# Optimization experiments

Hardware: AMD Instinct MI355X
Metric: run time of the kernel (lower is better)

The kernel has to match this reference:

```python
import jax, jax.numpy as jnp
import numpy as np

N_PED = 131072      # total pedestrians (batch)
SEG = 64            # pedestrians per segment (equal-size groups)
N_SEQ = N_PED // SEG
D_IN = 256          # enc_h_dim
D_OUT = 128         # mlp_dim


def setup_inputs() -> dict:
    key = jax.random.key(0)
    k1, k2 = jax.random.split(key, 2)
    h_states = jax.random.normal(k1, (N_PED, D_IN), dtype=jnp.float32)
    W = jax.random.normal(k2, (D_IN, D_OUT), dtype=jnp.float32) * 0.05
    b = jnp.zeros((D_OUT,), dtype=jnp.float32)
    starts = jnp.arange(N_SEQ, dtype=jnp.int64) * SEG
    seq_start_end = jnp.stack([starts, starts + SEG], axis=1)  # [N_SEQ, 2]
    return {"h_states": h_states, "W": W, "b": b, "seq_start_end": seq_start_end}


def reference(h_states, W, b, seq_start_end):
    # fc projection: (N, D_IN) -> (N, D_OUT)
    h = h_states @ W + b
    # gather each segment: equal-size groups of SEG pedestrians
    starts = seq_start_end[:, 0]                     # [G]
    idx = starts[:, None] + jnp.arange(SEG)[None, :]  # [G, S]
    seg = h[idx]                                      # [G, S, D_OUT]
    # per-segment self-attention pooling: softmax(H H^T) @ H
    scores = jnp.einsum('gsd,gtd->gst', seg, seg)     # [G, S, S]
    attn = jax.nn.softmax(scores, axis=-1)
    ctx = jnp.einsum('gst,gtd->gsd', attn, seg)       # [G, S, D_OUT]
    return ctx.reshape(-1, D_OUT)                     # [N, D_OUT]
```

## Files before the change

kernel.cpp:

```cpp
#include <hip/hip_runtime.h>
#include <stdint.h>

#define SEG 64
#define D_IN 256
#define D_OUT 128
#define NSEQ 2048

typedef __attribute__((ext_vector_type(8))) _Float16 half8;
typedef __attribute__((ext_vector_type(4))) float floatx4;

static __device__ __forceinline__ unsigned short f2h_bits(float f) {
  union { _Float16 h; unsigned short u; } v; v.h = (_Float16)f; return v.u;
}

__global__ void prep_w_kernel(const float* __restrict__ W,
                              unsigned short* __restrict__ Wf) {
  const int idx = blockIdx.x * 256 + threadIdx.x;
  const float v = W[idx];
  const int k = idx >> 7, n = idx & 127;
  const int slot = (((n >> 4) * 8 + (k >> 5)) * 64 + ((n & 15) + 16 * ((k >> 3) & 3))) * 8 + (k & 7);
  Wf[slot] = f2h_bits(v);
}

struct SharedHT {
  unsigned short h[4][4][64][8];
  unsigned short ht[8][2][64][8];
};
union alignas(16) SharedU {
  unsigned short a[4][8][64][8];
  SharedHT s;
};

__global__ __launch_bounds__(256, 4)
void attn_fused(const float* __restrict__ hs,
                const unsigned short* __restrict__ Wf,
                const float* __restrict__ bias,
                float* __restrict__ out)
{
  __shared__ SharedU u;
  __shared__ float rowinv[SEG];

  const int g    = blockIdx.x;
  const int tid  = (int)threadIdx.x;
  const int w    = tid >> 6;
  const int lane = tid & 63;
  const int c    = lane & 15;
  const int q    = lane >> 4;

  {
    const float4* gsrc = (const float4*)(hs + (size_t)g * (SEG * D_IN));
#pragma unroll
    for (int i = 0; i < 16; ++i) {
      const int f = i * 256 + tid;
      const float4 v = gsrc[f];
      const int row = f >> 6, col0 = (f & 63) * 4;
      const unsigned lo = (unsigned)f2h_bits(v.x) | ((unsigned)f2h_bits(v.y) << 16);
      const unsigned hi = (unsigned)f2h_bits(v.z) | ((unsigned)f2h_bits(v.w) << 16);
      *(uint2*)(&u.a[row >> 4][col0 >> 5][(row & 15) + 16 * ((col0 >> 3) & 3)][col0 & 7]) =
          make_uint2(lo, hi);
    }
  }

  float bv[2];
#pragma unroll
  for (int nt = 0; nt < 2; ++nt) bv[nt] = bias[(2 * w + nt) * 16 + c];
  floatx4 acc[2][4];
#pragma unroll
  for (int nt = 0; nt < 2; ++nt)
#pragma unroll
    for (int mt = 0; mt < 4; ++mt)
      acc[nt][mt] = (floatx4){bv[nt], bv[nt], bv[nt], bv[nt]};

  __syncthreads();

  {
    const half8* WfV = (const half8*)Wf;
#pragma unroll
    for (int ks = 0; ks < 8; ++ks) {
      const half8 wf0 = WfV[((2 * w + 0) * 8 + ks) * 64 + lane];
      const half8 wf1 = WfV[((2 * w + 1) * 8 + ks) * 64 + lane];
      half8 af[4];
#pragma unroll
      for (int mt = 0; mt < 4; ++mt)
        af[mt] = *(const half8*)(&u.a[mt][ks][lane][0]);
#pragma unroll
      for (int mt = 0; mt < 4; ++mt) {
        acc[0][mt] = __builtin_amdgcn_mfma_f32_16x16x32_f16(af[mt], wf0, acc[0][mt], 0, 0, 0);
        acc[1][mt] = __builtin_amdgcn_mfma_f32_16x16x32_f16(af[mt], wf1, acc[1][mt], 0, 0, 0);
      }
    }
  }

  __syncthreads();

#pragma unroll
  for (int nt = 0; nt < 2; ++nt) {
    const int ntg = 2 * w + nt;
#pragma unroll
    for (int mt = 0; mt < 4; ++mt) {
      unsigned short hb[4];
#pragma unroll
      for (int i = 0; i < 4; ++i) hb[i] = f2h_bits(acc[nt][mt][i]);
      const int lph = 16 * ((2 * nt + (c >> 3)) & 3);
#pragma unroll
      for (int i = 0; i < 4; ++i)
        u.s.h[mt][w][4 * q + i + lph][c & 7] = hb[i];
      const int lanep = c + 16 * ((2 * mt + (q >> 1)) & 3);
      const unsigned lo = (unsigned)hb[0] | ((unsigned)hb[1] << 16);
      const unsigned hi = (unsigned)hb[2] | ((unsigned)hb[3] << 16);
      *(uint2*)(&u.s.ht[ntg][mt >> 1][lanep][(q & 1) * 4]) = make_uint2(lo, hi);
    }
  }

  __syncthreads();

  floatx4 sacc[4];
#pragma unroll
  for (int nt = 0; nt < 4; ++nt) sacc[nt] = (floatx4){0.f, 0.f, 0.f, 0.f};
#pragma unroll
  for (int ks = 0; ks < 4; ++ks) {
    const half8 a = *(const half8*)(&u.s.h[w][ks][lane][0]);
#pragma unroll
    for (int nt = 0; nt < 4; ++nt) {
      const half8 b = *(const half8*)(&u.s.h[nt][ks][lane][0]);
      sacc[nt] = __builtin_amdgcn_mfma_f32_16x16x32_f16(a, b, sacc[nt], 0, 0, 0);
    }
  }

  __syncthreads();

  unsigned short pb[4][4];
  float rs[4];
#pragma unroll
  for (int i = 0; i < 4; ++i) {
    float m = fmaxf(fmaxf(sacc[0][i], sacc[1][i]), fmaxf(sacc[2][i], sacc[3][i]));
#pragma unroll
    for (int d = 1; d < 16; d <<= 1) m = fmaxf(m, __shfl_xor(m, d, 64));
    float ssum = 0.f;
#pragma unroll
    for (int nt = 0; nt < 4; ++nt) {
      const float e = __expf(sacc[nt][i] - m);
      ssum += e;
      pb[i][nt] = f2h_bits(e);
    }
#pragma unroll
    for (int d = 1; d < 16; d <<= 1) ssum += __shfl_xor(ssum, d, 64);
    rs[i] = ssum;
  }

  unsigned short (*pfr)[2][64][8] = (unsigned short(*)[2][64][8])(&u.s.h[0][0][0][0]);
#pragma unroll
  for (int i = 0; i < 4; ++i)
#pragma unroll
    for (int nt = 0; nt < 4; ++nt)
      pfr[w][nt >> 1][4 * q + i + 16 * ((2 * nt + (c >> 3)) & 3)][c & 7] = pb[i][nt];
  if (c == 0) {
#pragma unroll
    for (int i = 0; i < 4; ++i)
      rowinv[16 * w + 4 * q + i] = 1.0f / rs[i];
  }

  __syncthreads();

  floatx4 cacc[4][2];
#pragma unroll
  for (int mt = 0; mt < 4; ++mt)
#pragma unroll
    for (int nn = 0; nn < 2; ++nn) cacc[mt][nn] = (floatx4){0.f, 0.f, 0.f, 0.f};
#pragma unroll
  for (int ks = 0; ks < 2; ++ks) {
    half8 bfr[2];
#pragma unroll
    for (int nn = 0; nn < 2; ++nn)
      bfr[nn] = *(const half8*)(&u.s.ht[2 * w + nn][ks][lane][0]);
#pragma unroll
    for (int mt = 0; mt < 4; ++mt) {
      const half8 a = *(const half8*)(&pfr[mt][ks][lane][0]);
#pragma unroll
      for (int nn = 0; nn < 2; ++nn)
        cacc[mt][nn] = __builtin_amdgcn_mfma_f32_16x16x32_f16(a, bfr[nn], cacc[mt][nn], 0, 0, 0);
    }
  }

  float* ob = out + (size_t)g * (SEG * D_OUT);
#pragma unroll
  for (int mt = 0; mt < 4; ++mt)
#pragma unroll
    for (int i = 0; i < 4; ++i) {
      const int s = 16 * mt + 4 * q + i;
      const float inv = rowinv[s];
#pragma unroll
      for (int nn = 0; nn < 2; ++nn)
        ob[s * D_OUT + 32 * w + 16 * nn + c] = cacc[mt][nn][i] * inv;
    }
}

extern "C" void kernel_launch(void* const* d_in, const int* in_sizes, int n_in,
                              void* d_out, int out_size, void* d_ws, size_t ws_size,
                              hipStream_t stream) {
  const float* hs   = (const float*)d_in[0];
  const float* W    = (const float*)d_in[1];
  const float* bias = (const float*)d_in[2];
  float* out = (float*)d_out;
  unsigned short* Wf = (unsigned short*)d_ws;

  prep_w_kernel<<<128, 256, 0, stream>>>(W, Wf);
  attn_fused<<<NSEQ, 256, 0, stream>>>(hs, Wf, bias, out);
}
```

Before: 222.5 us.

## Remove two barriers by keeping P@V per-wave with private softmax buffer

Each wave now does the P@V product for its own 16 query rows across all 128 output columns, using a private per-wave probability buffer. That removes the two block barriers around the softmax write and the rowinv array, and normalization is folded into the probabilities before the fp16 conversion. The input load is restructured so each thread loads four consecutive float4 values and writes 16-byte LDS stores, and the first W fragment is prefetched before the barrier. The cost is an extra 4KB of LDS and rounding the normalized probabilities to fp16, which shifts numerics slightly. The output stores also change pattern.

```diff
diff --git a/kernel.cpp b/kernel.cpp
--- a/kernel.cpp
+++ b/kernel.cpp
@@ -11,6 +11,9 @@
 
 static __device__ __forceinline__ unsigned short f2h_bits(float f) {
   union { _Float16 h; unsigned short u; } v; v.h = (_Float16)f; return v.u;
+}
+static __device__ __forceinline__ unsigned pack2(float a, float b) {
+  return (unsigned)f2h_bits(a) | ((unsigned)f2h_bits(b) << 16);
 }
 
 __global__ void prep_w_kernel(const float* __restrict__ W,
@@ -38,7 +41,7 @@
                 float* __restrict__ out)
 {
   __shared__ SharedU u;
-  __shared__ float rowinv[SEG];
+  __shared__ unsigned short pbuf[4][2][64][8];
 
   const int g    = blockIdx.x;
   const int tid  = (int)threadIdx.x;
@@ -50,16 +53,29 @@
   {
     const float4* gsrc = (const float4*)(hs + (size_t)g * (SEG * D_IN));
 #pragma unroll
-    for (int i = 0; i < 16; ++i) {
-      const int f = i * 256 + tid;
-      const float4 v = gsrc[f];
-      const int row = f >> 6, col0 = (f & 63) * 4;
-      const unsigned lo = (unsigned)f2h_bits(v.x) | ((unsigned)f2h_bits(v.y) << 16);
-      const unsigned hi = (unsigned)f2h_bits(v.z) | ((unsigned)f2h_bits(v.w) << 16);
-      *(uint2*)(&u.a[row >> 4][col0 >> 5][(row & 15) + 16 * ((col0 >> 3) & 3)][col0 & 7]) =
-          make_uint2(lo, hi);
-    }
-  }
+    for (int i = 0; i < 4; ++i) {
+      const int qb = i * 1024 + tid * 4;
+      const float4 v0 = gsrc[qb + 0];
+      const float4 v1 = gsrc[qb + 1];
+      const float4 v2 = gsrc[qb + 2];
+      const float4 v3 = gsrc[qb + 3];
+      const int row  = i * 16 + (tid >> 4);
+      const int ks   = (tid & 15) >> 1;
+      const int slot = (row & 15) + ((tid & 1) << 5);
+      unsigned short* d0 = &u.a[row >> 4][ks][slot][0];
+      uint4 wa, wb;
+      wa.x = pack2(v0.x, v0.y); wa.y = pack2(v0.z, v0.w);
+      wa.z = pack2(v1.x, v1.y); wa.w = pack2(v1.z, v1.w);
+      wb.x = pack2(v2.x, v2.y); wb.y = pack2(v2.z, v2.w);
+      wb.z = pack2(v3.x, v3.y); wb.w = pack2(v3.z, v3.w);
+      *(uint4*)d0         = wa;
+      *(uint4*)(d0 + 128) = wb;
+    }
+  }
+
+  const half8* WfV = (const half8*)Wf;
+  const half8 wpre0 = WfV[((2 * w + 0) * 8 + 0) * 64 + lane];
+  const half8 wpre1 = WfV[((2 * w + 1) * 8 + 0) * 64 + lane];
 
   float bv[2];
 #pragma unroll
@@ -73,21 +89,18 @@
 
   __syncthreads();
 
-  {
-    const half8* WfV = (const half8*)Wf;
-#pragma unroll
-    for (int ks = 0; ks < 8; ++ks) {
-      const half8 wf0 = WfV[((2 * w + 0) * 8 + ks) * 64 + lane];
-      const half8 wf1 = WfV[((2 * w + 1) * 8 + ks) * 64 + lane];
-      half8 af[4];
-#pragma unroll
-      for (int mt = 0; mt < 4; ++mt)
-        af[mt] = *(const half8*)(&u.a[mt][ks][lane][0]);
-#pragma unroll
-      for (int mt = 0; mt < 4; ++mt) {
-        acc[0][mt] = __builtin_amdgcn_mfma_f32_16x16x32_f16(af[mt], wf0, acc[0][mt], 0, 0, 0);
-        acc[1][mt] = __builtin_amdgcn_mfma_f32_16x16x32_f16(af[mt], wf1, acc[1][mt], 0, 0, 0);
-      }
+#pragma unroll
+  for (int ks = 0; ks < 8; ++ks) {
+    const half8 wf0 = ks ? WfV[((2 * w + 0) * 8 + ks) * 64 + lane] : wpre0;
+    const half8 wf1 = ks ? WfV[((2 * w + 1) * 8 + ks) * 64 + lane] : wpre1;
+    half8 af[4];
+#pragma unroll
+    for (int mt = 0; mt < 4; ++mt)
+      af[mt] = *(const half8*)(&u.a[mt][ks][lane][0]);
+#pragma unroll
+    for (int mt = 0; mt < 4; ++mt) {
+      acc[0][mt] = __builtin_amdgcn_mfma_f32_16x16x32_f16(af[mt], wf0, acc[0][mt], 0, 0, 0);
+      acc[1][mt] = __builtin_amdgcn_mfma_f32_16x16x32_f16(af[mt], wf1, acc[1][mt], 0, 0, 0);
     }
   }
 
@@ -127,10 +140,8 @@
     }
   }
 
-  __syncthreads();
-
-  unsigned short pb[4][4];
-  float rs[4];
+  float ev[4][4];
+  float inv[4];
 #pragma unroll
   for (int i = 0; i < 4; ++i) {
     float m = fmaxf(fmaxf(sacc[0][i], sacc[1][i]), fmaxf(sacc[2][i], sacc[3][i]));
@@ -139,60 +150,40 @@
     float ssum = 0.f;
 #pragma unroll
     for (int nt = 0; nt < 4; ++nt) {
-      const float e = __expf(sacc[nt][i] - m);
-      ssum += e;
-      pb[i][nt] = f2h_bits(e);
+      ev[i][nt] = __expf(sacc[nt][i] - m);
+      ssum += ev[i][nt];
     }
 #pragma unroll
     for (int d = 1; d < 16; d <<= 1) ssum += __shfl_xor(ssum, d, 64);
-    rs[i] = ssum;
-  }
-
-  unsigned short (*pfr)[2][64][8] = (unsigned short(*)[2][64][8])(&u.s.h[0][0][0][0]);
+    inv[i] = 1.0f / ssum;
+  }
+
 #pragma unroll
   for (int i = 0; i < 4; ++i)
 #pragma unroll
     for (int nt = 0; nt < 4; ++nt)
-      pfr[w][nt >> 1][4 * q + i + 16 * ((2 * nt + (c >> 3)) & 3)][c & 7] = pb[i][nt];
-  if (c == 0) {
-#pragma unroll
-    for (int i = 0; i < 4; ++i)
-      rowinv[16 * w + 4 * q + i] = 1.0f / rs[i];
-  }
-
-  __syncthreads();
-
-  floatx4 cacc[4][2];
-#pragma unroll
-  for (int mt = 0; mt < 4; ++mt)
-#pragma unroll
-    for (int nn = 0; nn < 2; ++nn) cacc[mt][nn] = (floatx4){0.f, 0.f, 0.f, 0.f};
-#pragma unroll
-  for (int ks = 0; ks < 2; ++ks) {
-    half8 bfr[2];
-#pragma unroll
-    for (int nn = 0; nn < 2; ++nn)
-      bfr[nn] = *(const half8*)(&u.s.ht[2 * w + nn][ks][lane][0]);
-#pragma unroll
-    for (int mt = 0; mt < 4; ++mt) {
-      const half8 a = *(const half8*)(&pfr[mt][ks][lane][0]);
-#pragma unroll
-      for (int nn = 0; nn < 2; ++nn)
-        cacc[mt][nn] = __builtin_amdgcn_mfma_f32_16x16x32_f16(a, bfr[nn], cacc[mt][nn], 0, 0, 0);
-    }
-  }
-
-  float* ob = out + (size_t)g * (SEG * D_OUT);
-#pragma unroll
-  for (int mt = 0; mt < 4; ++mt)
-#pragma unroll
-    for (int i = 0; i < 4; ++i) {
-      const int s = 16 * mt + 4 * q + i;
-      const float inv = rowinv[s];
-#pragma unroll
-      for (int nn = 0; nn < 2; ++nn)
-        ob[s * D_OUT + 32 * w + 16 * nn + c] = cacc[mt][nn][i] * inv;
-    }
+      pbuf[w][nt >> 1][4 * q + i + 16 * ((2 * nt + (c >> 3)) & 3)][c & 7] =
+          f2h_bits(ev[i][nt] * inv[i]);
+
+  floatx4 cacc[8];
+#pragma unroll
+  for (int nt = 0; nt < 8; ++nt) cacc[nt] = (floatx4){0.f, 0.f, 0.f, 0.f};
+#pragma unroll
+  for (int kt = 0; kt < 2; ++kt) {
+    const half8 a = *(const half8*)(&pbuf[w][kt][lane][0]);
+#pragma unroll
+    for (int nt = 0; nt < 8; ++nt) {
+      const half8 b = *(const half8*)(&u.s.ht[nt][kt][lane][0]);
+      cacc[nt] = __builtin_amdgcn_mfma_f32_16x16x32_f16(a, b, cacc[nt], 0, 0, 0);
+    }
+  }
+
+  float* ob = out + (size_t)g * (SEG * D_OUT) + (size_t)(16 * w + 4 * q) * D_OUT + c;
+#pragma unroll
+  for (int i = 0; i < 4; ++i)
+#pragma unroll
+    for (int nt = 0; nt < 8; ++nt)
+      ob[i * D_OUT + 16 * nt] = cacc[nt][i];
 }
 
 extern "C" void kernel_launch(void* const* d_in, const int* in_sizes, int n_in,
```

Measured after the change: 220.8 us. Within noise of the previous version (-0.8%).
